# Optimization experiments

Measured on AMD Instinct MI355X. Metric: run time of the kernel, lower is better.

## Reference

```python
import jax, jax.numpy as jnp
import numpy as np

B, S, D_MODEL, N_HEADS = 4, 2048, 512, 2
D4 = D_MODEL * 4            # output dim of quaternion projections (2048)
HD = D4 // N_HEADS          # per-head dim (1024)
EPS = 1e-6


def quat_linear(x, W, b):
    """Hamilton-product quaternion linear.
    x: [..., 4*in_q] (quaternions interleaved r,i,j,k)
    W: [4, out_q, in_q] components (r,i,j,k); b: [4*out_q]
    returns [..., 4*out_q]
    """
    xq = x.reshape(x.shape[:-1] + (-1, 4))
    xr, xi, xj, xk = xq[..., 0], xq[..., 1], xq[..., 2], xq[..., 3]
    Wr, Wi, Wj, Wk = W[0], W[1], W[2], W[3]
    m = lambda a, M: jnp.einsum('...i,oi->...o', a, M)
    o_r = m(xr, Wr) - m(xi, Wi) - m(xj, Wj) - m(xk, Wk)
    o_i = m(xr, Wi) + m(xi, Wr) + m(xj, Wk) - m(xk, Wj)
    o_j = m(xr, Wj) - m(xi, Wk) + m(xj, Wr) + m(xk, Wi)
    o_k = m(xr, Wk) + m(xi, Wj) - m(xj, Wi) + m(xk, Wr)
    out = jnp.stack([o_r, o_i, o_j, o_k], axis=-1)
    return out.reshape(out.shape[:-2] + (-1,)) + b


def setup_inputs() -> dict:
    rng = jax.random.key(0)
    ks = jax.random.split(rng, 12)
    def w(k, out_q, in_q):
        return jax.random.normal(k, (4, out_q, in_q), jnp.float32) * (1.0 / np.sqrt(4.0 * in_q))
    in_q_small = D_MODEL // 4   # q/k/v projections: d_model reals -> d_model quaternions
    in_q_big = D4 // 4          # later projections: 4*d_model reals -> d_model quaternions
    zb = jnp.zeros((D4,), jnp.float32)
    return {
        'query': jax.random.normal(ks[0], (B, S, D_MODEL), jnp.float32),
        'key':   jax.random.normal(ks[1], (B, S, D_MODEL), jnp.float32),
        'value': jax.random.normal(ks[2], (B, S, D_MODEL), jnp.float32),
        'Wq': w(ks[3], D_MODEL, in_q_small), 'bq': zb,
        'Wk': w(ks[4], D_MODEL, in_q_small), 'bk': zb,
        'Wv': w(ks[5], D_MODEL, in_q_small), 'bv': zb,
        'alpha': jax.random.normal(ks[6], (D4,), jnp.float32) * 0.1,
        'Wint': w(ks[7], D_MODEL, in_q_big), 'bint': zb,
        'Wfin': w(ks[8], D_MODEL, in_q_big), 'bfin': zb,
        'Wout': w(ks[9], D_MODEL, in_q_big), 'bout': zb,
    }


def reference(query, key, value, Wq, bq, Wk, bk, Wv, bv, alpha,
              Wint, bint, Wfin, bfin, Wout, bout):
    Q = quat_linear(query, Wq, bq).reshape(B, S, N_HEADS, HD)
    K = quat_linear(key, Wk, bk).reshape(B, S, N_HEADS, HD)
    V = quat_linear(value, Wv, bv).reshape(B, S, N_HEADS, HD)

    # spectral attention: FFT correlation + adaptive spectral filter
    Qf = jnp.fft.fft(Q, axis=1)
    Kf = jnp.fft.fft(K, axis=1)
    corr = Qf * jnp.conj(Kf)                        # [B,S,H,HD] complex64
    freqs = jnp.abs(jnp.fft.fftfreq(S))             # [S]
    phase = jnp.arctan(jnp.log(freqs + EPS))        # [S]
    a = alpha.reshape(N_HEADS, HD)
    filt = jnp.exp(1j * (phase[:, None, None] * a[None, :, :]))  # [S,H,HD]
    attn_w = jnp.fft.ifft(corr * filt[None], axis=1).real        # [B,S,H,HD]
    attn = (attn_w * V).reshape(B, S, -1)           # [B,S,4*d_model]

    attn = quat_linear(attn, Wint, bint)
    attn = quat_linear(attn, Wfin, bfin)
    return quat_linear(attn, Wout, bout)            # [B,S,4*d_model]
```

## Files before the change

### kernel.cpp

```cpp
#include <hip/hip_runtime.h>
#include <hip/hip_bf16.h>
#include <cstdint>

typedef unsigned short u16;
typedef u16  u16x4 __attribute__((ext_vector_type(4)));
typedef u16  u16x8 __attribute__((ext_vector_type(8)));
typedef short s16x8 __attribute__((ext_vector_type(8)));
typedef float f32x4 __attribute__((ext_vector_type(4)));

#define PI_F 3.14159265358979323846f
#define PD(i) ((i) + 3 * ((i) >> 5))

static __device__ __forceinline__ u16 f2bf(float f) {
    union { float f; unsigned u; } v; v.f = f;
    unsigned r = v.u + 0x7fffu + ((v.u >> 16) & 1u);
    return (u16)(r >> 16);
}
static __device__ __forceinline__ float bf2f(u16 h) {
    union { unsigned u; float f; } v; v.u = ((unsigned)h) << 16;
    return v.f;
}

__device__ __forceinline__ void gl_lds16(const u16* g, u16* l) {
    __builtin_amdgcn_global_load_lds(
        (const __attribute__((address_space(1))) unsigned int*)g,
        (__attribute__((address_space(3))) unsigned int*)l, 16, 0, 0);
}

__device__ __forceinline__ void cvt_body(int blk, const float* __restrict__ in,
                                         u16* __restrict__ o) {
    int i = blk * 256 + threadIdx.x;
    float4 a = ((const float4*)in)[2 * i];
    float4 b = ((const float4*)in)[2 * i + 1];
    u16x8 vv;
    vv[0] = f2bf(a.x); vv[1] = f2bf(a.y); vv[2] = f2bf(a.z); vv[3] = f2bf(a.w);
    vv[4] = f2bf(b.x); vv[5] = f2bf(b.y); vv[6] = f2bf(b.z); vv[7] = f2bf(b.w);
    ((u16x8*)o)[i] = vv;
}

__device__ __forceinline__ void hamilton(int c, int cp, int& qmv, float& qsv) {
    const int   qm[4][4] = {{0,1,2,3},{1,0,3,2},{2,3,0,1},{3,2,1,0}};
    const float qs[4][4] = {{1.f,-1.f,-1.f,-1.f},{1.f,1.f,1.f,-1.f},
                            {1.f,-1.f,1.f,1.f},{1.f,1.f,-1.f,1.f}};
    qmv = qm[c][cp]; qsv = qs[c][cp];
}

template<int LOGK>
__device__ __forceinline__ void e3_body(int blk, const float* __restrict__ W,
                                        u16* __restrict__ E) {
    const int K = 1 << LOGK;
    int idx = blk * 256 + threadIdx.x;
    int n = idx >> LOGK, k = idx & (K - 1);
    int o = n >> 2, c = n & 3, i = k >> 2, cp = k & 3;
    int qmv; float qsv; hamilton(c, cp, qmv, qsv);
    int in_q = K >> 2;
    float w = W[(size_t)qmv * 512 * in_q + (size_t)o * in_q + i] * qsv;
    E[idx] = f2bf(w);
}

__device__ __forceinline__ void e3t_body(int blk, const float* __restrict__ W,
                                         u16* __restrict__ ET) {
    int idx = blk * 256 + threadIdx.x;
    int k = idx >> 11, n = idx & 2047;
    int o = n >> 2, c = n & 3, i = k >> 2, cp = k & 3;
    int qmv; float qsv; hamilton(c, cp, qmv, qsv);
    float w = W[(size_t)qmv * 512 * 512 + (size_t)o * 512 + i] * qsv;
    ET[idx] = f2bf(w);
}

__device__ __forceinline__ void tabs_body(int blk, float2* __restrict__ gws,
                                          float* __restrict__ ph) {
    int i = blk * 256 + threadIdx.x;
    if (i < 292) {
        int off, denom;
        if (i < 4)       { off = 0;  denom = 16;   }
        else if (i < 36) { off = 4;  denom = 128;  }
        else             { off = 36; denom = 1024; }
        float a = (-PI_F) * (float)(i - off) / (float)denom;
        gws[i] = make_float2(cosf(a), sinf(a));
    }
    if (i <= 1024) {
        ph[i] = atanf(logf((float)i * (1.0f / 2048.0f) + 1e-6f));
    }
}

__global__ __launch_bounds__(256) void fat_prep(
        const float* __restrict__ query, const float* __restrict__ key,
        const float* __restrict__ value, u16* __restrict__ Acvt,
        const float* __restrict__ Wq, const float* __restrict__ Wk,
        const float* __restrict__ Wv, u16* __restrict__ Eq,
        u16* __restrict__ Ek, u16* __restrict__ Ev,
        const float* __restrict__ Wint, const float* __restrict__ Wfin,
        const float* __restrict__ Wout, u16* __restrict__ EintT,
        u16* __restrict__ Efin, u16* __restrict__ Eout,
        float2* __restrict__ gws, float* __restrict__ pht) {
    int b = blockIdx.x;
    if (b < 6144) {
        int ten = b >> 11, r = b & 2047;
        const float* in = (ten == 0) ? query : (ten == 1) ? key : value;
        cvt_body(r, in, Acvt + (size_t)ten * 8192 * 512);
    } else if (b < 18432) {
        int rb = b - 6144;
        int y = rb >> 12, r = rb & 4095;
        e3_body<9>(r, (y == 0) ? Wq : (y == 1) ? Wk : Wv,
                   (y == 0) ? Eq : (y == 1) ? Ek : Ev);
    } else if (b < 34816) {
        e3t_body(b - 18432, Wint, EintT);
    } else if (b < 51200) {
        e3_body<11>(b - 34816, Wfin, Efin);
    } else if (b < 67584) {
        e3_body<11>(b - 51200, Wout, Eout);
    } else {
        tabs_body(b - 67584, gws, pht);
    }
}

__device__ __forceinline__ void mv_body(int blk, const float* __restrict__ v,
                                        const u16* __restrict__ E,
                                        const float* __restrict__ badd,
                                        float* __restrict__ out) {
    int n    = (blk * 256 + threadIdx.x) >> 6;
    int lane = threadIdx.x & 63;
    if (n >= 2048) return;
    const u16* row = E + (size_t)n * 2048;
    float s = 0.f;
    for (int j = lane; j < 2048; j += 64) s += v[j] * bf2f(row[j]);
#pragma unroll
    for (int o = 32; o; o >>= 1) s += __shfl_down(s, o, 64);
    if (lane == 0) out[n] = s + badd[n];
}

template<int K, int OUTMODE, int NBY>
__device__ __forceinline__ void gemm_body(int bid, u16* As, u16* Bs,
                                          const u16* __restrict__ A,
                                          const u16* __restrict__ E,
                                          const float* __restrict__ bias,
                                          void* __restrict__ outp) {
    const int t    = threadIdx.x;
    const int lane = t & 63, wave = t >> 6;
    const int wr   = wave >> 1, wc = wave & 1;
    const int lr   = lane & 15, kg = lane >> 4;
    const int l7   = lr & 7;

    constexpr int SPX = (4 * (NBY / 4)) / 8;
    const int xcd = bid & 7, p = bid >> 3;
    const int st  = xcd * SPX + (p >> 4);
    const int w   = p & 15;
    const int bx  = (st & 3) * 4 + (w & 3);
    const int by  = (st >> 2) * 4 + (w >> 2);
    const int m0  = by * 128;
    const int n0  = bx * 128;

    f32x4 acc[4][4];
#pragma unroll
    for (int i = 0; i < 4; ++i)
#pragma unroll
        for (int j = 0; j < 4; ++j) acc[i][j] = (f32x4){0.f, 0.f, 0.f, 0.f};

    const int arow = wr * 64 + lr;
    const int brow = wc * 64 + lr;

    for (int k0 = 0; k0 < K; k0 += 64) {
#pragma unroll
        for (int c = 0; c < 4; ++c) {
            int idx = t + c * 256;
            int row = idx >> 3, sl = idx & 7;
            int gsl = sl ^ (row & 7);
            gl_lds16(A + (size_t)(m0 + row) * K + k0 + gsl * 8, &As[idx * 8]);
            gl_lds16(E + (size_t)(n0 + row) * K + k0 + gsl * 8, &Bs[idx * 8]);
        }
        __syncthreads();
#pragma unroll
        for (int ks = 0; ks < 2; ++ks) {
            const int slot = (ks * 4 + kg) ^ l7;
            s16x8 av[4], bv[4];
#pragma unroll
            for (int mi = 0; mi < 4; ++mi)
                av[mi] = *(const s16x8*)&As[(arow + mi * 16) * 64 + slot * 8];
#pragma unroll
            for (int ni = 0; ni < 4; ++ni)
                bv[ni] = *(const s16x8*)&Bs[(brow + ni * 16) * 64 + slot * 8];
#pragma unroll
            for (int mi = 0; mi < 4; ++mi)
#pragma unroll
                for (int ni = 0; ni < 4; ++ni)
                    acc[mi][ni] = __builtin_amdgcn_mfma_f32_16x16x32_bf16(
                        av[mi], bv[ni], acc[mi][ni], 0, 0, 0);
        }
        __syncthreads();
    }

#pragma unroll
    for (int ni = 0; ni < 4; ++ni) {
        int n = n0 + wc * 64 + ni * 16 + lr;
        float bvl = bias ? bias[n] : 0.0f;
#pragma unroll
        for (int mi = 0; mi < 4; ++mi) {
#pragma unroll
            for (int r = 0; r < 4; ++r) {
                int m = m0 + wr * 64 + mi * 16 + kg * 4 + r;
                float val = acc[mi][ni][r] + bvl;
                if constexpr (OUTMODE == 0) {
                    ((u16*)outp)[(size_t)m * 2048 + n] = f2bf(val);
                } else if constexpr (OUTMODE == 1) {
                    ((float*)outp)[(size_t)m * 2048 + n] = val;
                } else {
                    int b = m >> 11, s = m & 2047;
                    ((u16*)outp)[((size_t)b * 2048 + n) * 2048 + s] = f2bf(val);
                }
            }
        }
    }
}

template<int K, int OUTMODE, int NBY>
__global__ __launch_bounds__(256) void gemm2(const u16* __restrict__ A,
                                             const u16* __restrict__ E,
                                             const float* __restrict__ bias,
                                             void* __restrict__ outp) {
    __shared__ u16 As[128 * 64];
    __shared__ u16 Bs[128 * 64];
    gemm_body<K, OUTMODE, NBY>(blockIdx.x, As, Bs, A, E, bias, outp);
}

__global__ __launch_bounds__(256) void gemm_fatA(const u16* __restrict__ Aq,
                                                 const u16* __restrict__ Eq,
                                                 const float* __restrict__ bq,
                                                 void* __restrict__ Qt,
                                                 const u16* __restrict__ Ak,
                                                 const u16* __restrict__ Ek,
                                                 const float* __restrict__ bk,
                                                 void* __restrict__ Kt,
                                                 const u16* __restrict__ Efin,
                                                 const u16* __restrict__ EintT,
                                                 void* __restrict__ T1T,
                                                 const float* __restrict__ bint,
                                                 const float* __restrict__ bfin,
                                                 float* __restrict__ bv1) {
    __shared__ u16 As[128 * 64];
    __shared__ u16 Bs[128 * 64];
    int bid = blockIdx.x;
    if (bid < 256) {
        gemm_body<2048, 2, 16>(bid, As, Bs, Efin, EintT, nullptr, T1T);
    } else if (bid < 1280) {
        gemm_body<512, 2, 64>(bid - 256, As, Bs, Aq, Eq, bq, Qt);
    } else if (bid < 2304) {
        gemm_body<512, 2, 64>(bid - 1280, As, Bs, Ak, Ek, bk, Kt);
    } else {
        mv_body(bid - 2304, bint, Efin, bfin, bv1);
    }
}

template<int LH, int OFF>
__device__ __forceinline__ void r8pass(float* re, float* im,
                                       const float2* __restrict__ wt, int t) {
    constexpr int h = 1 << LH;
    __syncthreads();
    const int j  = t & (h - 1);
    const int i0 = ((t >> LH) << (LH + 3)) | j;
    const float2 w = wt[OFF + j];
    const float t2r = w.x * w.x - w.y * w.y;
    const float t2i = 2.f * w.x * w.y;
    const float t1r = t2r * t2r - t2i * t2i;
    const float t1i = 2.f * t2r * t2i;
    const float S = 0.70710678118654752f;
    const float Ac = S * (w.x + w.y);
    const float Bc = S * (w.y - w.x);

    float xr[8], xi[8];
    int p[8];
#pragma unroll
    for (int k = 0; k < 8; ++k) {
        p[k] = PD(i0 + k * h);
        xr[k] = re[p[k]]; xi[k] = im[p[k]];
    }
#pragma unroll
    for (int kp = 0; kp < 8; kp += 2) {
        float tr = t1r * xr[kp + 1] - t1i * xi[kp + 1];
        float ti = t1r * xi[kp + 1] + t1i * xr[kp + 1];
        float ar = xr[kp], ai = xi[kp];
        xr[kp] = ar + tr;     xi[kp] = ai + ti;
        xr[kp + 1] = ar - tr; xi[kp + 1] = ai - ti;
    }
#pragma unroll
    for (int q = 0; q < 2; ++q) {
        int b0 = q * 4;
        {
            float tr = t2r * xr[b0 + 2] - t2i * xi[b0 + 2];
            float ti = t2r * xi[b0 + 2] + t2i * xr[b0 + 2];
            float ar = xr[b0], ai = xi[b0];
            xr[b0] = ar + tr;     xi[b0] = ai + ti;
            xr[b0 + 2] = ar - tr; xi[b0 + 2] = ai - ti;
        }
        {
            float tr = t2i * xr[b0 + 3] + t2r * xi[b0 + 3];
            float ti = t2i * xi[b0 + 3] - t2r * xr[b0 + 3];
            float ar = xr[b0 + 1], ai = xi[b0 + 1];
            xr[b0 + 1] = ar + tr; xi[b0 + 1] = ai + ti;
            xr[b0 + 3] = ar - tr; xi[b0 + 3] = ai - ti;
        }
    }
    {
        float tr = w.x * xr[4] - w.y * xi[4];
        float ti = w.x * xi[4] + w.y * xr[4];
        float ar = xr[0], ai = xi[0];
        xr[0] = ar + tr; xi[0] = ai + ti;
        xr[4] = ar - tr; xi[4] = ai - ti;
    }
    {
        float tr = Ac * xr[5] - Bc * xi[5];
        float ti = Ac * xi[5] + Bc * xr[5];
        float ar = xr[1], ai = xi[1];
        xr[1] = ar + tr; xi[1] = ai + ti;
        xr[5] = ar - tr; xi[5] = ai - ti;
    }
    {
        float tr = w.y * xr[6] + w.x * xi[6];
        float ti = w.y * xi[6] - w.x * xr[6];
        float ar = xr[2], ai = xi[2];
        xr[2] = ar + tr; xi[2] = ai + ti;
        xr[6] = ar - tr; xi[6] = ai - ti;
    }
    {
        float tr = Bc * xr[7] + Ac * xi[7];
        float ti = Bc * xi[7] - Ac * xr[7];
        float ar = xr[3], ai = xi[3];
        xr[3] = ar + tr; xi[3] = ai + ti;
        xr[7] = ar - tr; xi[7] = ai - ti;
    }
#pragma unroll
    for (int k = 0; k < 8; ++k) { re[p[k]] = xr[k]; im[p[k]] = xi[k]; }
}

__device__ void fft2048(float* re, float* im, const float2* __restrict__ wt, int t) {
    __syncthreads();
#pragma unroll
    for (int u = 0; u < 2; ++u) {
        int i0 = (t + u * 256) << 2;
        int p0 = PD(i0);
        float x0r = re[p0],     x0i = im[p0];
        float x1r = re[p0 + 1], x1i = im[p0 + 1];
        float x2r = re[p0 + 2], x2i = im[p0 + 2];
        float x3r = re[p0 + 3], x3i = im[p0 + 3];
        float ar = x0r + x1r, ai = x0i + x1i;
        float br = x0r - x1r, bi = x0i - x1i;
        float cr = x2r + x3r, ci = x2i + x3i;
        float dr = x2r - x3r, di = x2i - x3i;
        re[p0]     = ar + cr; im[p0]     = ai + ci;
        re[p0 + 2] = ar - cr; im[p0 + 2] = ai - ci;
        re[p0 + 1] = br + di; im[p0 + 1] = bi - dr;
        re[p0 + 3] = br - di; im[p0 + 3] = bi + dr;
    }
    r8pass<2, 0>(re, im, wt, t);
    r8pass<5, 4>(re, im, wt, t);
    r8pass<8, 36>(re, im, wt, t);
    __syncthreads();
}

__device__ void spectral_body(int sbid, float* zre, float* zim, float2* wt,
                              const u16* __restrict__ Qt,
                              const u16* __restrict__ Kt,
                              u16* __restrict__ Wt,
                              const float* __restrict__ alpha,
                              const float2* __restrict__ gws,
                              const float* __restrict__ gph) {
    const int t  = threadIdx.x;
    const int b  = sbid >> 10;
    const int cp = sbid & 1023;
    const int c0 = cp * 2;
    const size_t base0 = ((size_t)b * 2048 + c0) * 2048;
    const size_t base1 = base0 + 2048;

    for (int i = t; i < 292; i += 256) wt[i] = gws[i];

    float ph[4];
    float PH1r[4], PH1i[4], PH2r[4], PH2i[4];
    float ph24 = 0.f, PH24_1 = 0.f, PH24_2 = 0.f;

#pragma unroll
    for (int ch = 0; ch < 2; ++ch) {
        const size_t base = ch ? base1 : base0;
        const u16* Qp = Qt + base;
        const u16* Kp = Kt + base;
        __syncthreads();
#pragma unroll
        for (int u = 0; u < 8; ++u) {
            int s = t + u * 256;
            int r = __brev((unsigned)s) >> 21;
            zre[PD(r)] = bf2f(Qp[s]);
            zim[PD(r)] = bf2f(Kp[s]);
        }
        fft2048(zre, zim, wt, t);
        const float ac = alpha[c0 + ch];
#pragma unroll
        for (int u = 0; u < 4; ++u) {
            int k = t + u * 256;
            int m = (2048 - k) & 2047;
            float ar = zre[PD(k)], ai = zim[PD(k)];
            float br = zre[PD(m)], bi = zim[PD(m)];
            float qr = 0.5f * (ar + br), qi = 0.5f * (ai - bi);
            float kr = 0.5f * (ai + bi), ki = 0.5f * (br - ar);
            float cr = qr * kr + qi * ki;
            float ci = qi * kr - qr * ki;
            if (ch == 0) ph[u] = gph[min(k, 2048 - k)];
            float fr, fi;
            __sincosf(ph[u] * ac, &fi, &fr);
            float Pkr = cr * fr - ci * fi, Pki = cr * fi + ci * fr;
            float qr2 = 0.5f * (br + ar), qi2 = 0.5f * (bi - ai);
            float kr2 = 0.5f * (bi + ai), ki2 = 0.5f * (ar - br);
            float cr2 = qr2 * kr2 + qi2 * ki2;
            float ci2 = qi2 * kr2 - qr2 * ki2;
            float Pmr = cr2 * fr - ci2 * fi, Pmi = cr2 * fi + ci2 * fr;
            float hr = 0.5f * (Pkr + Pmr), hi = 0.5f * (Pki - Pmi);
            if (ch == 0) { PH1r[u] = hr; PH1i[u] = hi; }
            else         { PH2r[u] = hr; PH2i[u] = hi; }
        }
        if (t == 0) {
            float ar = zre[PD(1024)], ai = zim[PD(1024)];
            float cr = ar * ai;
            if (ch == 0) ph24 = gph[1024];
            float fr, fi;
            __sincosf(ph24 * ac, &fi, &fr);
            if (ch == 0) PH24_1 = cr * fr; else PH24_2 = cr * fr;
        }
    }

    __syncthreads();
#pragma unroll
    for (int u = 0; u < 4; ++u) {
        int k = t + u * 256;
        int m = (2048 - k) & 2047;
        int rk = __brev((unsigned)k) >> 21;
        int rm = __brev((unsigned)m) >> 21;
        zre[PD(rk)] = PH1r[u] - PH2i[u];
        zim[PD(rk)] = PH1i[u] + PH2r[u];
        zre[PD(rm)] = PH1r[u] + PH2i[u];
        zim[PD(rm)] = PH2r[u] - PH1i[u];
    }
    if (t == 0) {
        zre[PD(1)] = PH24_1;
        zim[PD(1)] = PH24_2;
    }
    fft2048(zre, zim, wt, t);

#pragma unroll
    for (int u = 0; u < 8; ++u) {
        int s = t + u * 256;
        int j = (2048 - s) & 2047;
        Wt[base0 + s] = f2bf(zre[PD(j)] * (1.0f / 2048.0f));
        Wt[base1 + s] = f2bf(zim[PD(j)] * (1.0f / 2048.0f));
    }
}

__global__ __launch_bounds__(256) void fat_specv(const u16* __restrict__ Qt,
                                                 const u16* __restrict__ Kt,
                                                 u16* __restrict__ Wt,
                                                 const float* __restrict__ alpha,
                                                 const float2* __restrict__ gws,
                                                 const float* __restrict__ gph,
                                                 const u16* __restrict__ Av,
                                                 const u16* __restrict__ Ev,
                                                 const float* __restrict__ bvb,
                                                 void* __restrict__ Vt,
                                                 const u16* __restrict__ Eout,
                                                 const u16* __restrict__ T1T,
                                                 void* __restrict__ Ecomb,
                                                 const float* __restrict__ bv1,
                                                 const float* __restrict__ bout,
                                                 float* __restrict__ bv2) {
    __shared__ __align__(16) char smem[32768];
    int bid = blockIdx.x;
    if (bid < 256) {
        gemm_body<2048, 0, 16>(bid, (u16*)smem, (u16*)(smem + 16384),
                               Eout, T1T, nullptr, Ecomb);
        return;
    }
    if (bid >= 5376) {
        mv_body(bid - 5376, bv1, Eout, bout, bv2);
        return;
    }
    bid -= 256;
    if (bid % 5 == 4) {
        gemm_body<512, 2, 64>(bid / 5, (u16*)smem, (u16*)(smem + 16384),
                              Av, Ev, bvb, Vt);
    } else {
        int sbid = (bid / 5) * 4 + (bid % 5);
        spectral_body(sbid, (float*)smem, (float*)(smem + 8960),
                      (float2*)(smem + 17920), Qt, Kt, Wt, alpha, gws, gph);
    }
}

__global__ __launch_bounds__(256) void transpose_mul(const u16* __restrict__ W,
                                                     const u16* __restrict__ V,
                                                     u16* __restrict__ out) {
    __shared__ u16 tile[64][70];
    const int b  = blockIdx.z;
    const int c0 = blockIdx.x * 64, s0 = blockIdx.y * 64;
    const int t  = threadIdx.x;
    const int g  = (t & 15) * 4;
    const int rb = t >> 4;

#pragma unroll
    for (int r = 0; r < 4; ++r) {
        int c = rb + 16 * r;
        size_t idx = ((size_t)b * 2048 + c0 + c) * 2048 + s0 + g;
        u16x4 wv = *(const u16x4*)&W[idx];
        u16x4 vv = *(const u16x4*)&V[idx];
#pragma unroll
        for (int j = 0; j < 4; ++j)
            tile[c][g + j] = f2bf(bf2f(wv[j]) * bf2f(vv[j]));
    }
    __syncthreads();
#pragma unroll
    for (int r = 0; r < 4; ++r) {
        int s = rb + 16 * r;
        u16x4 o;
#pragma unroll
        for (int j = 0; j < 4; ++j) o[j] = tile[g + j][s];
        *(u16x4*)&out[((size_t)b * 2048 + s0 + s) * 2048 + c0 + g] = o;
    }
}

extern "C" void kernel_launch(void* const* d_in, const int* in_sizes, int n_in,
                              void* d_out, int out_size, void* d_ws, size_t ws_size,
                              hipStream_t stream) {
    const float* query = (const float*)d_in[0];
    const float* key   = (const float*)d_in[1];
    const float* value = (const float*)d_in[2];
    const float* Wq    = (const float*)d_in[3];
    const float* bq    = (const float*)d_in[4];
    const float* Wk    = (const float*)d_in[5];
    const float* bk    = (const float*)d_in[6];
    const float* Wv    = (const float*)d_in[7];
    const float* bv    = (const float*)d_in[8];
    const float* alpha = (const float*)d_in[9];
    const float* Wint  = (const float*)d_in[10];
    const float* bint  = (const float*)d_in[11];
    const float* Wfin  = (const float*)d_in[12];
    const float* bfin  = (const float*)d_in[13];
    const float* Wout  = (const float*)d_in[14];
    const float* bout  = (const float*)d_in[15];

    char* ws = (char*)d_ws;
    size_t off = 0;
    auto alloc = [&](size_t bytes) -> void* {
        void* p = ws + off;
        off += (bytes + 255) & ~(size_t)255;
        return p;
    };
    u16* Eq   = (u16*)alloc((size_t)2048 * 512 * 2);
    u16* Ek   = (u16*)alloc((size_t)2048 * 512 * 2);
    u16* Ev   = (u16*)alloc((size_t)2048 * 512 * 2);
    u16* Ecomb= (u16*)alloc((size_t)2048 * 2048 * 2);
    u16* Efin = (u16*)alloc((size_t)2048 * 2048 * 2);
    u16* Eout = (u16*)alloc((size_t)2048 * 2048 * 2);
    u16* EintT= (u16*)alloc((size_t)2048 * 2048 * 2);
    u16* T1T  = (u16*)alloc((size_t)2048 * 2048 * 2);
    u16* Qt   = (u16*)alloc((size_t)4 * 2048 * 2048 * 2);
    u16* Kt   = (u16*)alloc((size_t)4 * 2048 * 2048 * 2);
    u16* Vt   = (u16*)alloc((size_t)4 * 2048 * 2048 * 2);
    u16* attn = (u16*)alloc((size_t)8192 * 2048 * 2);
    float2* gws = (float2*)alloc(292 * 8);
    float*  pht = (float*)alloc(1025 * 4);
    float*  bv1 = (float*)alloc(2048 * 4);
    float*  bv2 = (float*)alloc(2048 * 4);
    u16* Wt    = Qt;
    u16* Aq = attn;
    u16* Ak = attn + (size_t)8192 * 512;
    u16* Av = attn + (size_t)8192 * 1024;

    fat_prep<<<67589, 256, 0, stream>>>(query, key, value, Aq,
                                        Wq, Wk, Wv, Eq, Ek, Ev,
                                        Wint, Wfin, Wout, EintT, Efin, Eout,
                                        gws, pht);

    gemm_fatA<<<2816, 256, 0, stream>>>(Aq, Eq, bq, Qt, Ak, Ek, bk, Kt,
                                        Efin, EintT, T1T, bint, bfin, bv1);

    fat_specv<<<5888, 256, 0, stream>>>(Qt, Kt, Wt, alpha, gws, pht,
                                        Av, Ev, bv, Vt, Eout, T1T, Ecomb,
                                        bv1, bout, bv2);

    dim3 gt(32, 32, 4);
    transpose_mul<<<gt, 256, 0, stream>>>(Wt, Vt, attn);

    gemm2<2048, 1, 64><<<1024, 256, 0, stream>>>(attn, Ecomb, bv2, (float*)d_out);
}
```

Measured before the change: 353.9 us.

## Combine quaternion weight products in compact component form before expanding

The three trailing quaternion projections were folded into one combined 2048x2048 matrix by multiplying full expanded bf16 weight matrices (K=2048 GEMMs). This change multiplies the raw component weights with K=512 GEMMs, recombines the 4x4 component products with Hamilton sign rules in small qcomb kernels, and expands to the full matrix only at the end. That removes most of the weight-expansion traffic and GEMM FLOPs in prep. In exchange it adds a kernel launch (qcomb1), merges the transpose-multiply into a fat_post kernel, and computes the bias matvecs directly from fp32 weights.

```diff
diff --git a/kernel.cpp b/kernel.cpp
--- a/kernel.cpp
+++ b/kernel.cpp
@@ -58,14 +58,12 @@
     E[idx] = f2bf(w);
 }
 
-__device__ __forceinline__ void e3t_body(int blk, const float* __restrict__ W,
-                                         u16* __restrict__ ET) {
-    int idx = blk * 256 + threadIdx.x;
-    int k = idx >> 11, n = idx & 2047;
-    int o = n >> 2, c = n & 3, i = k >> 2, cp = k & 3;
-    int qmv; float qsv; hamilton(c, cp, qmv, qsv);
-    float w = W[(size_t)qmv * 512 * 512 + (size_t)o * 512 + i] * qsv;
-    ET[idx] = f2bf(w);
+__device__ __forceinline__ void ytr_body(int blk, const float* __restrict__ W,
+                                         u16* __restrict__ YT) {
+    int b = blk * 256 + threadIdx.x;
+    int row = b >> 9, o = b & 511;
+    int cb = row >> 9, i = row & 511;
+    YT[b] = f2bf(W[((size_t)cb * 512 + o) * 512 + i]);
 }
 
 __device__ __forceinline__ void tabs_body(int blk, float2* __restrict__ gws,
@@ -91,8 +89,8 @@
         const float* __restrict__ Wv, u16* __restrict__ Eq,
         u16* __restrict__ Ek, u16* __restrict__ Ev,
         const float* __restrict__ Wint, const float* __restrict__ Wfin,
-        const float* __restrict__ Wout, u16* __restrict__ EintT,
-        u16* __restrict__ Efin, u16* __restrict__ Eout,
+        const float* __restrict__ Wout, u16* __restrict__ Xfin,
+        u16* __restrict__ Xout, u16* __restrict__ YtInt,
         float2* __restrict__ gws, float* __restrict__ pht) {
     int b = blockIdx.x;
     if (b < 6144) {
@@ -104,29 +102,33 @@
         int y = rb >> 12, r = rb & 4095;
         e3_body<9>(r, (y == 0) ? Wq : (y == 1) ? Wk : Wv,
                    (y == 0) ? Eq : (y == 1) ? Ek : Ev);
-    } else if (b < 34816) {
-        e3t_body(b - 18432, Wint, EintT);
-    } else if (b < 51200) {
-        e3_body<11>(b - 34816, Wfin, Efin);
-    } else if (b < 67584) {
-        e3_body<11>(b - 51200, Wout, Eout);
+    } else if (b < 18944) {
+        cvt_body(b - 18432, Wfin, Xfin);
+    } else if (b < 19456) {
+        cvt_body(b - 18944, Wout, Xout);
+    } else if (b < 23552) {
+        ytr_body(b - 19456, Wint, YtInt);
     } else {
-        tabs_body(b - 67584, gws, pht);
-    }
-}
-
-__device__ __forceinline__ void mv_body(int blk, const float* __restrict__ v,
-                                        const u16* __restrict__ E,
-                                        const float* __restrict__ badd,
-                                        float* __restrict__ out) {
+        tabs_body(b - 23552, gws, pht);
+    }
+}
+
+__device__ __forceinline__ void mvW_body(int blk, const float* __restrict__ v,
+                                         const float* __restrict__ W,
+                                         const float* __restrict__ badd,
+                                         float* __restrict__ out) {
     int n    = (blk * 256 + threadIdx.x) >> 6;
     int lane = threadIdx.x & 63;
     if (n >= 2048) return;
-    const u16* row = E + (size_t)n * 2048;
+    int o = n >> 2, c = n & 3;
+    int cp = lane & 3;
+    int qmv; float qsv; hamilton(c, cp, qmv, qsv);
+    const float* Wrow = W + ((size_t)qmv * 512 + o) * 512;
     float s = 0.f;
-    for (int j = lane; j < 2048; j += 64) s += v[j] * bf2f(row[j]);
-#pragma unroll
-    for (int o = 32; o; o >>= 1) s += __shfl_down(s, o, 64);
+    for (int k = lane; k < 2048; k += 64) s += v[k] * Wrow[k >> 2];
+    s *= qsv;
+#pragma unroll
+    for (int off = 32; off; off >>= 1) s += __shfl_down(s, off, 64);
     if (lane == 0) out[n] = s + badd[n];
 }
 
@@ -231,9 +233,10 @@
                                                  const u16* __restrict__ Ek,
                                                  const float* __restrict__ bk,
                                                  void* __restrict__ Kt,
-                                                 const u16* __restrict__ Efin,
-                                                 const u16* __restrict__ EintT,
-                                                 void* __restrict__ T1T,
+                                                 const u16* __restrict__ Xfin,
+                                                 const u16* __restrict__ YtInt,
+                                                 void* __restrict__ Z1,
+                                                 const float* __restrict__ Wfin,
                                                  const float* __restrict__ bint,
                                                  const float* __restrict__ bfin,
                                                  float* __restrict__ bv1) {
@@ -241,14 +244,41 @@
     __shared__ u16 Bs[128 * 64];
     int bid = blockIdx.x;
     if (bid < 256) {
-        gemm_body<2048, 2, 16>(bid, As, Bs, Efin, EintT, nullptr, T1T);
+        gemm_body<512, 0, 16>(bid, As, Bs, Xfin, YtInt, nullptr, Z1);
     } else if (bid < 1280) {
         gemm_body<512, 2, 64>(bid - 256, As, Bs, Aq, Eq, bq, Qt);
     } else if (bid < 2304) {
         gemm_body<512, 2, 64>(bid - 1280, As, Bs, Ak, Ek, bk, Kt);
     } else {
-        mv_body(bid - 2304, bint, Efin, bfin, bv1);
-    }
+        mvW_body(bid - 2304, bint, Wfin, bfin, bv1);
+    }
+}
+
+__global__ __launch_bounds__(256) void qcomb1(const u16* __restrict__ Z1,
+                                              u16* __restrict__ Yt2) {
+    __shared__ float tile[32][33];
+    const int CA[4][4] = {{0,1,2,3},{1,0,3,2},{2,0,1,3},{3,0,2,1}};
+    const int CB[4][4] = {{0,1,2,3},{0,1,2,3},{0,2,3,1},{0,3,1,2}};
+    const float SG[4][4] = {{1.f,-1.f,-1.f,-1.f},{1.f,1.f,1.f,-1.f},
+                            {1.f,1.f,1.f,-1.f},{1.f,1.f,1.f,-1.f}};
+    const int cm = blockIdx.z;
+    const int p0 = blockIdx.x * 32, i0 = blockIdx.y * 32;
+    const int tx = threadIdx.x, ty = threadIdx.y;
+#pragma unroll
+    for (int dy = 0; dy < 32; dy += 8) {
+        int p = p0 + ty + dy;
+        float acc = 0.f;
+#pragma unroll
+        for (int q = 0; q < 4; ++q)
+            acc += SG[cm][q] * bf2f(Z1[(size_t)(CA[cm][q] * 512 + p) * 2048
+                                       + CB[cm][q] * 512 + i0 + tx]);
+        tile[ty + dy][tx] = acc;
+    }
+    __syncthreads();
+#pragma unroll
+    for (int dy = 0; dy < 32; dy += 8)
+        Yt2[((size_t)cm * 512 + i0 + ty + dy) * 512 + p0 + tx]
+            = f2bf(tile[tx][ty + dy]);
 }
 
 template<int LH, int OFF>
@@ -462,21 +492,22 @@
                                                  const u16* __restrict__ Ev,
                                                  const float* __restrict__ bvb,
                                                  void* __restrict__ Vt,
-                                                 const u16* __restrict__ Eout,
-                                                 const u16* __restrict__ T1T,
-                                                 void* __restrict__ Ecomb,
+                                                 const u16* __restrict__ Xout,
+                                                 const u16* __restrict__ Yt2,
+                                                 void* __restrict__ Z2,
+                                                 const float* __restrict__ Wout,
                                                  const float* __restrict__ bv1,
                                                  const float* __restrict__ bout,
                                                  float* __restrict__ bv2) {
     __shared__ __align__(16) char smem[32768];
     int bid = blockIdx.x;
     if (bid < 256) {
-        gemm_body<2048, 0, 16>(bid, (u16*)smem, (u16*)(smem + 16384),
-                               Eout, T1T, nullptr, Ecomb);
+        gemm_body<512, 0, 16>(bid, (u16*)smem, (u16*)(smem + 16384),
+                              Xout, Yt2, nullptr, Z2);
         return;
     }
     if (bid >= 5376) {
-        mv_body(bid - 5376, bv1, Eout, bout, bv2);
+        mvW_body(bid - 5376, bv1, Wout, bout, bv2);
         return;
     }
     bid -= 256;
@@ -490,16 +521,42 @@
     }
 }
 
-__global__ __launch_bounds__(256) void transpose_mul(const u16* __restrict__ W,
-                                                     const u16* __restrict__ V,
-                                                     u16* __restrict__ out) {
-    __shared__ u16 tile[64][70];
-    const int b  = blockIdx.z;
-    const int c0 = blockIdx.x * 64, s0 = blockIdx.y * 64;
+__device__ __forceinline__ void qcomb2_body(int blk, const u16* __restrict__ Z2,
+                                            u16* __restrict__ Ecomb) {
+    int id = blk * 256 + threadIdx.x;
+    int q = id >> 9, i = id & 511;
+    float z[4][4];
+#pragma unroll
+    for (int ca = 0; ca < 4; ++ca)
+#pragma unroll
+        for (int cb = 0; cb < 4; ++cb)
+            z[ca][cb] = bf2f(Z2[(size_t)(ca * 512 + q) * 2048 + cb * 512 + i]);
+    float wc[4];
+    wc[0] = z[0][0] - z[1][1] - z[2][2] - z[3][3];
+    wc[1] = z[1][0] + z[0][1] + z[3][2] - z[2][3];
+    wc[2] = z[2][0] + z[0][2] + z[1][3] - z[3][1];
+    wc[3] = z[3][0] + z[0][3] + z[2][1] - z[1][2];
+#pragma unroll
+    for (int c = 0; c < 4; ++c) {
+        u16x4 row;
+#pragma unroll
+        for (int cp = 0; cp < 4; ++cp) {
+            int qmv; float qsv; hamilton(c, cp, qmv, qsv);
+            row[cp] = f2bf(qsv * wc[qmv]);
+        }
+        *(u16x4*)&Ecomb[(size_t)(4 * q + c) * 2048 + 4 * i] = row;
+    }
+}
+
+__device__ __forceinline__ void tmul_body(int blk, const u16* __restrict__ W,
+                                          const u16* __restrict__ V,
+                                          u16* __restrict__ out, u16* tile) {
+    const int b  = blk >> 10;
+    const int rem = blk & 1023;
+    const int c0 = (rem & 31) * 64, s0 = (rem >> 5) * 64;
     const int t  = threadIdx.x;
     const int g  = (t & 15) * 4;
     const int rb = t >> 4;
-
 #pragma unroll
     for (int r = 0; r < 4; ++r) {
         int c = rb + 16 * r;
@@ -508,7 +565,7 @@
         u16x4 vv = *(const u16x4*)&V[idx];
 #pragma unroll
         for (int j = 0; j < 4; ++j)
-            tile[c][g + j] = f2bf(bf2f(wv[j]) * bf2f(vv[j]));
+            tile[c * 70 + g + j] = f2bf(bf2f(wv[j]) * bf2f(vv[j]));
     }
     __syncthreads();
 #pragma unroll
@@ -516,9 +573,20 @@
         int s = rb + 16 * r;
         u16x4 o;
 #pragma unroll
-        for (int j = 0; j < 4; ++j) o[j] = tile[g + j][s];
+        for (int j = 0; j < 4; ++j) o[j] = tile[(g + j) * 70 + s];
         *(u16x4*)&out[((size_t)b * 2048 + s0 + s) * 2048 + c0 + g] = o;
     }
+}
+
+__global__ __launch_bounds__(256) void fat_post(const u16* __restrict__ Z2,
+                                                u16* __restrict__ Ecomb,
+                                                const u16* __restrict__ W,
+                                                const u16* __restrict__ V,
+                                                u16* __restrict__ attn) {
+    __shared__ u16 tile[64 * 70];
+    int bid = blockIdx.x;
+    if (bid < 1024) qcomb2_body(bid, Z2, Ecomb);
+    else            tmul_body(bid - 1024, W, V, attn, tile);
 }
 
 extern "C" void kernel_launch(void* const* d_in, const int* in_sizes, int n_in,
@@ -548,41 +616,44 @@
         off += (bytes + 255) & ~(size_t)255;
         return p;
     };
-    u16* Eq   = (u16*)alloc((size_t)2048 * 512 * 2);
-    u16* Ek   = (u16*)alloc((size_t)2048 * 512 * 2);
-    u16* Ev   = (u16*)alloc((size_t)2048 * 512 * 2);
-    u16* Ecomb= (u16*)alloc((size_t)2048 * 2048 * 2);
-    u16* Efin = (u16*)alloc((size_t)2048 * 2048 * 2);
-    u16* Eout = (u16*)alloc((size_t)2048 * 2048 * 2);
-    u16* EintT= (u16*)alloc((size_t)2048 * 2048 * 2);
-    u16* T1T  = (u16*)alloc((size_t)2048 * 2048 * 2);
-    u16* Qt   = (u16*)alloc((size_t)4 * 2048 * 2048 * 2);
-    u16* Kt   = (u16*)alloc((size_t)4 * 2048 * 2048 * 2);
-    u16* Vt   = (u16*)alloc((size_t)4 * 2048 * 2048 * 2);
-    u16* attn = (u16*)alloc((size_t)8192 * 2048 * 2);
+    u16* Eq    = (u16*)alloc((size_t)2048 * 512 * 2);
+    u16* Ek    = (u16*)alloc((size_t)2048 * 512 * 2);
+    u16* Ev    = (u16*)alloc((size_t)2048 * 512 * 2);
+    u16* Xfin  = (u16*)alloc((size_t)2048 * 512 * 2);
+    u16* Xout  = (u16*)alloc((size_t)2048 * 512 * 2);
+    u16* YtInt = (u16*)alloc((size_t)2048 * 512 * 2);
+    u16* Yt2   = (u16*)alloc((size_t)2048 * 512 * 2);
+    u16* Z1    = (u16*)alloc((size_t)2048 * 2048 * 2);
+    u16* Z2    = (u16*)alloc((size_t)2048 * 2048 * 2);
+    u16* Ecomb = (u16*)alloc((size_t)2048 * 2048 * 2);
+    u16* Qt    = (u16*)alloc((size_t)4 * 2048 * 2048 * 2);
+    u16* Kt    = (u16*)alloc((size_t)4 * 2048 * 2048 * 2);
+    u16* Vt    = (u16*)alloc((size_t)4 * 2048 * 2048 * 2);
+    u16* attn  = (u16*)alloc((size_t)8192 * 2048 * 2);
     float2* gws = (float2*)alloc(292 * 8);
     float*  pht = (float*)alloc(1025 * 4);
     float*  bv1 = (float*)alloc(2048 * 4);
     float*  bv2 = (float*)alloc(2048 * 4);
-    u16* Wt    = Qt;
+    u16* Wt = Qt;
     u16* Aq = attn;
     u16* Ak = attn + (size_t)8192 * 512;
     u16* Av = attn + (size_t)8192 * 1024;
 
-    fat_prep<<<67589, 256, 0, stream>>>(query, key, value, Aq,
+    fat_prep<<<23557, 256, 0, stream>>>(query, key, value, Aq,
                                         Wq, Wk, Wv, Eq, Ek, Ev,
-                                        Wint, Wfin, Wout, EintT, Efin, Eout,
+                                        Wint, Wfin, Wout, Xfin, Xout, YtInt,
                                         gws, pht);
 
     gemm_fatA<<<2816, 256, 0, stream>>>(Aq, Eq, bq, Qt, Ak, Ek, bk, Kt,
-                                        Efin, EintT, T1T, bint, bfin, bv1);
+                                        Xfin, YtInt, Z1, Wfin, bint, bfin, bv1);
+
+    qcomb1<<<dim3(16, 16, 4), dim3(32, 8), 0, stream>>>(Z1, Yt2);
 
     fat_specv<<<5888, 256, 0, stream>>>(Qt, Kt, Wt, alpha, gws, pht,
-                                        Av, Ev, bv, Vt, Eout, T1T, Ecomb,
-                                        bv1, bout, bv2);
-
-    dim3 gt(32, 32, 4);
-    transpose_mul<<<gt, 256, 0, stream>>>(Wt, Vt, attn);
+                                        Av, Ev, bv, Vt, Xout, Yt2, Z2,
+                                        Wout, bv1, bout, bv2);
+
+    fat_post<<<5120, 256, 0, stream>>>(Z2, Ecomb, Wt, Vt, attn);
 
     gemm2<2048, 1, 64><<<1024, 256, 0, stream>>>(attn, Ecomb, bv2, (float*)d_out);
 }
```

After: 306.7 us, median of 2. 13.3% less time.
